# Kernel tuning notes

Measured on AMD Instinct MI355X. Metric: run time of the kernel, lower is better.

## Reference

```python
import jax, jax.numpy as jnp
import numpy as np

NBINS = 16  # init_kwargs nBins


def _next_fast_len(n):
    # smallest 5-smooth integer >= n (matches FastCMIF._nextFastLen)
    while True:
        m = n
        for p in (2, 3, 5):
            while m % p == 0:
                m //= p
        if m == 1:
            return n
        n += 1


def _normalize(im):
    mn = jnp.min(im, axis=(-2, -1), keepdims=True)
    mx = jnp.max(im, axis=(-2, -1), keepdims=True)
    return (im - mn) / (mx - mn)


def _one_hot(im):
    # (..., H, W) -> (..., NBINS, H, W)
    q = jnp.floor(im * (NBINS - 1)).astype(jnp.int32)
    return jnp.moveaxis(jax.nn.one_hot(q, NBINS, dtype=jnp.float32), -1, -3)


def _fftconv(im, template, padWl, padHt):
    s = (_next_fast_len(im.shape[-2] + template.shape[-2] - 1),
         _next_fast_len(im.shape[-1] + template.shape[-1] - 1))
    F = jnp.fft.rfft2(im, s=s) * jnp.fft.rfft2(jnp.flip(template, (-2, -1)), s=s)
    out = jnp.fft.irfft2(F, s=s)
    return out[..., padHt:padHt + im.shape[-2], padWl:padWl + im.shape[-1]]


def setup_inputs() -> dict:
    key = jax.random.key(0)
    k1, k2 = jax.random.split(key)
    im = jax.random.uniform(k1, (2, 1, 384, 384), dtype=jnp.float32)
    template = jax.random.uniform(k2, (2, 1, 48, 48), dtype=jnp.float32)
    return {"im": im, "template": template}


def reference(im, template):
    padWl = (template.shape[-1] - 1) // 2
    padHt = (template.shape[-2] - 1) // 2
    imOh = _one_hot(_normalize(im))            # (B,C,nBins,H,W)
    tOh = _one_hot(_normalize(template))       # (B,C,nBins,h,w)
    # marginal sliding-window histograms
    Px = _fftconv(imOh, jnp.ones_like(tOh), padWl, padHt)
    Py = _fftconv(jnp.ones_like(imOh), tOh, padWl, padHt)
    N = jnp.sum(Px, axis=-3, keepdims=True)    # (B,C,1,H,W)
    # joint sliding-window histogram (B,C,nBins,nBins,H,W)
    Pxy = _fftconv(imOh[..., :, None, :, :], tOh[..., None, :, :, :], padWl, padHt)
    Pxy = Pxy / N[..., None, :, :, :]
    Px = Px / N
    Py = Py / N
    # norm == "none": masked KL(Pxy || Px*Py)
    PxPy = Px[..., :, None, :, :] * Py[..., None, :, :, :]
    mask = (Pxy > 0) & (PxPy > 0)
    term = Pxy * (jnp.log(jnp.where(mask, Pxy, 1.0)) - jnp.log(jnp.where(mask, PxPy, 1.0)))
    return jnp.sum(jnp.where(mask, term, 0.0), axis=(-4, -3))  # (B,C,H,W)
```

## Files before the change

### kernel.cpp

```cpp
#include <hip/hip_runtime.h>


#define IMH 384
#define IMW 384
#define TH 48
#define TW 48
#define PAD 24
#define PH 432
#define PIMG (PH*PH)
#define NIMGW (PIMG/4)
#define TOTW (2*NIMGW)
#define FLTMAX 3.402823466e+38f
#define LN2F 0.69314718055994530942f

#if __has_builtin(__builtin_amdgcn_alignbyte)
#define ALIGNBYTE(hi,lo,s) __builtin_amdgcn_alignbyte((hi),(lo),(s))
#else
#define ALIGNBYTE(hi,lo,s) ((unsigned)(((((unsigned long long)(hi))<<32)|(unsigned long long)(lo)) >> ((s)*8)))
#endif

__global__ void k_mm1(const float* __restrict__ im, const float* __restrict__ tm,
                      unsigned* __restrict__ mnmx) {
    int b = blockIdx.x;
    const float* src;
    int base, cnt, g;
    if (b < 64) { src = im + (b >> 5) * (IMH*IMW); base = (b & 31) * 4608; cnt = 4608; g = b >> 5; }
    else        { src = tm + ((b - 64) >> 1) * (TH*TW); base = ((b - 64) & 1) * 1152; cnt = 1152; g = 2 + ((b - 64) >> 1); }
    float mn0 = FLTMAX, mx0 = -FLTMAX, mn1 = FLTMAX, mx1 = -FLTMAX;
    for (int i = threadIdx.x; i < cnt; i += 512) {
        float v = src[base + i];
        mn0 = fminf(mn0, v); mx0 = fmaxf(mx0, v);
        if (i + 256 < cnt) {
            float w = src[base + i + 256];
            mn1 = fminf(mn1, w); mx1 = fmaxf(mx1, w);
        }
    }
    float mn = fminf(mn0, mn1), mx = fmaxf(mx0, mx1);
    for (int o = 32; o > 0; o >>= 1) {
        mn = fminf(mn, __shfl_down(mn, o));
        mx = fmaxf(mx, __shfl_down(mx, o));
    }
    __shared__ float smn[4], smx[4];
    int w = threadIdx.x >> 6;
    if ((threadIdx.x & 63) == 0) { smn[w] = mn; smx[w] = mx; }
    __syncthreads();
    if (threadIdx.x == 0) {
        mn = fminf(fminf(smn[0], smn[1]), fminf(smn[2], smn[3]));
        mx = fmaxf(fmaxf(smx[0], smx[1]), fmaxf(smx[2], smx[3]));
        atomicMin(&mnmx[g],     __float_as_uint(mn));
        atomicMax(&mnmx[4 + g], __float_as_uint(mx));
    }
}

__global__ void k_prep(const float* __restrict__ im, const float* __restrict__ tm,
                       const unsigned* __restrict__ mm,
                       unsigned* __restrict__ pImW, unsigned* __restrict__ pT) {
    int blk = blockIdx.x;
    if (blk < 365) {
        int wi = blk * 256 + threadIdx.x;
        if (wi >= TOTW) return;
        int b = wi / NIMGW;
        int rem4 = (wi - b * NIMGW) * 4;
        int py = rem4 / PH;
        int px = rem4 - py * PH;
        float mn = __uint_as_float(mm[b]), mx = __uint_as_float(mm[4 + b]);
        unsigned word = 0;
        #pragma unroll
        for (int j = 0; j < 4; ++j) {
            int x = px + j;
            unsigned bin = 16u;
            if (py >= PAD && py < PAD + IMH && x >= PAD && x < PAD + IMW) {
                float v = im[b * (IMH*IMW) + (py - PAD) * IMW + (x - PAD)];
                float r = (v - mn) / (mx - mn);
                bin = (unsigned)(int)floorf(r * 15.0f);
            }
            word |= bin << (8*j);
        }
        pImW[wi] = word;
    } else {
        for (int t = threadIdx.x; t < 576; t += 256) {
            int b = t / 288, w = t - b * 288;
            float mn = __uint_as_float(mm[2 + b]), mx = __uint_as_float(mm[6 + b]);
            const float* tptr = tm + b * (TH*TW) + w * 8;
            unsigned word = 0;
            #pragma unroll
            for (int j = 0; j < 8; ++j) {
                float r = (tptr[j] - mn) / (mx - mn);
                word |= ((unsigned)(int)floorf(r * 15.0f)) << (4*j);
            }
            pT[b*288 + w] = word;
        }
    }
}

__device__ __forceinline__ void load_row(const uint2* rowp, int r, unsigned (&w)[14]) {
    const uint2* p = rowp + r * (PH / 8);
    #pragma unroll
    for (int i = 0; i < 7; ++i) { uint2 v = p[i]; w[2*i] = v.x; w[2*i+1] = v.y; }
}
__device__ __forceinline__ void load_t(const uint2* tp, int r, unsigned (&t)[6]) {
    const uint2* p = tp + r * 3;
    #pragma unroll
    for (int i = 0; i < 3; ++i) { uint2 v = p[i]; t[2*i] = v.x; t[2*i+1] = v.y; }
}

template<bool BORDER>
__device__ __forceinline__ void do_row(const unsigned (&w)[14], const unsigned (&t)[6],
                                       unsigned* __restrict__ hist, int tid,
                                       unsigned sh, bool sel) {
    unsigned wsel[13];
    #pragma unroll
    for (int i = 0; i < 13; ++i) wsel[i] = sel ? w[i+1] : w[i];
    unsigned a[12];
    #pragma unroll
    for (int i = 0; i < 12; ++i) a[i] = ALIGNBYTE(wsel[i+1], wsel[i], sh);
    unsigned tq[6];
    #pragma unroll
    for (int j = 0; j < 6; ++j)
        tq[j] = (unsigned)__builtin_amdgcn_readfirstlane((int)t[j]);

    #pragma unroll
    for (int c = 0; c < 48; ++c) {
        unsigned byteval = (a[c >> 2] >> ((c & 3) * 8)) & 0xFFu;
        unsigned l    = (tq[c >> 3] >> ((c & 7) * 4)) & 0xFu;
        unsigned soff = (l >> 2) << 6;
        unsigned sadd = 1u << ((l & 3u) << 3);
        if (BORDER) {
            unsigned bin   = byteval & 15u;
            unsigned adder = (byteval != 16u) ? sadd : 0u;
            atomicAdd(&hist[(bin << 8) + soff + tid], adder);
        } else {
            atomicAdd(&hist[(byteval << 8) + soff + tid], sadd);
        }
    }
}

template<bool BORDER>
__device__ __forceinline__ void accum_tile(const uint2* rowp, const uint2* tp,
                                           unsigned* __restrict__ hist, int tid,
                                           unsigned sh, bool sel) {
    unsigned w0[14], w1[14], t0[6], t1[6];
    load_row(rowp, 0, w0); load_t(tp, 0, t0);
    #pragma unroll 1
    for (int r = 0; r < 12; r += 2) {
        load_row(rowp, r + 1, w1); load_t(tp, r + 1, t1);
        do_row<BORDER>(w0, t0, hist, tid, sh, sel);
        if (r + 2 < 12) { load_row(rowp, r + 2, w0); load_t(tp, r + 2, t0); }
        do_row<BORDER>(w1, t1, hist, tid, sh, sel);
    }
}

__global__ __launch_bounds__(256, 4)
void k_main(const unsigned char* __restrict__ pIm, const unsigned* __restrict__ pT,
            float* __restrict__ out) {
    __shared__ unsigned hist[16 * 4 * 64];
    const int wv  = threadIdx.x >> 6;
    const int tid = threadIdx.x & 63;
    const int tx = tid & 7, ty = tid >> 3;
    const int b = blockIdx.z;
    const int X0 = blockIdx.x << 3, Y0 = blockIdx.y << 3;

    {
        uint4 z = {0u, 0u, 0u, 0u};
        #pragma unroll
        for (int i = 0; i < 4; ++i) ((uint4*)hist)[(wv * 4 + i) * 64 + tid] = z;
    }
    __syncthreads();

    const uint2* rowp = (const uint2*)(pIm + b * PIMG + (Y0 + ty + 12 * wv) * PH + X0);
    const uint2* tp   = (const uint2*)(pT + b * 288) + wv * 36;
    const unsigned sh = tx & 3;
    const bool sel = (tx & 4) != 0;

    const bool interior = (blockIdx.x >= 3) && (blockIdx.x <= 43) &&
                          (blockIdx.y >= 3) && (blockIdx.y <= 43);
    if (interior) accum_tile<false>(rowp, tp, hist, tid, sh, sel);
    else          accum_tile<true >(rowp, tp, hist, tid, sh, sel);

    __syncthreads();
    if (wv != 0) return;

    float A = 0.0f;
    int coll[16];
    #pragma unroll
    for (int i = 0; i < 16; ++i) coll[i] = 0;
    int N = 0;
    #pragma unroll
    for (int k = 0; k < 16; ++k) {
        int rk = 0;
        #pragma unroll
        for (int q = 0; q < 4; ++q) {
            unsigned v = hist[(k << 8) + (q << 6) + tid];
            #pragma unroll
            for (int j = 0; j < 4; ++j) {
                int c = (int)((v >> (8*j)) & 0xFFu);
                rk += c;
                coll[(q << 2) + j] += c;
                if (c) A += (float)c * __log2f((float)c);
            }
        }
        if (rk) A -= (float)rk * __log2f((float)rk);
        N += rk;
    }
    #pragma unroll
    for (int i = 0; i < 16; ++i)
        if (coll[i]) A -= (float)coll[i] * __log2f((float)coll[i]);
    float fN = (float)N;
    out[(b * IMH + Y0 + ty) * IMW + X0 + tx] = (A + fN * __log2f(fN)) * LN2F / fN;
}

extern "C" void kernel_launch(void* const* d_in, const int* in_sizes, int n_in,
                              void* d_out, int out_size, void* d_ws, size_t ws_size,
                              hipStream_t stream) {
    const float* im = (const float*)d_in[0];
    const float* tm = (const float*)d_in[1];
    float* out = (float*)d_out;
    unsigned char* pIm = (unsigned char*)d_ws;
    unsigned* pT   = (unsigned*)((char*)d_ws + 373248);
    unsigned* mnmx = (unsigned*)((char*)d_ws + 375552);

    hipMemsetAsync(mnmx, 0x7f, 16, stream);
    hipMemsetAsync((char*)mnmx + 16, 0x00, 16, stream);
    k_mm1<<<68, 256, 0, stream>>>(im, tm, mnmx);
    k_prep<<<366, 256, 0, stream>>>(im, tm, mnmx, (unsigned*)pIm, pT);
    k_main<<<dim3(48, 48, 2), 256, 0, stream>>>(pIm, pT, out);
}
```

Before: 199.9 us.

## Split histogram epilogue across all waves and drop memsets in min/max pass

The final entropy reduction in the main kernel now spreads the 16 joint-histogram rows over all four waves instead of one. Each wave computes its partial log-sum and column sums, and wave 0 combines them through shared memory. This adds a barrier and extra shared-memory traffic but cuts the serial epilogue per block. The min/max kernel now uses one 1024-thread block per image with float4 loads and writes results directly, which removes the two memset launches and the atomics at the cost of less parallelism in that pass.

```diff
diff --git a/kernel.cpp b/kernel.cpp
--- a/kernel.cpp
+++ b/kernel.cpp
@@ -19,36 +19,39 @@
 #define ALIGNBYTE(hi,lo,s) ((unsigned)(((((unsigned long long)(hi))<<32)|(unsigned long long)(lo)) >> ((s)*8)))
 #endif
 
-__global__ void k_mm1(const float* __restrict__ im, const float* __restrict__ tm,
-                      unsigned* __restrict__ mnmx) {
+__global__ __launch_bounds__(1024)
+void k_mm1(const float* __restrict__ im, const float* __restrict__ tm,
+           unsigned* __restrict__ mnmx) {
     int b = blockIdx.x;
-    const float* src;
-    int base, cnt, g;
-    if (b < 64) { src = im + (b >> 5) * (IMH*IMW); base = (b & 31) * 4608; cnt = 4608; g = b >> 5; }
-    else        { src = tm + ((b - 64) >> 1) * (TH*TW); base = ((b - 64) & 1) * 1152; cnt = 1152; g = 2 + ((b - 64) >> 1); }
-    float mn0 = FLTMAX, mx0 = -FLTMAX, mn1 = FLTMAX, mx1 = -FLTMAX;
-    for (int i = threadIdx.x; i < cnt; i += 512) {
-        float v = src[base + i];
-        mn0 = fminf(mn0, v); mx0 = fmaxf(mx0, v);
-        if (i + 256 < cnt) {
-            float w = src[base + i + 256];
-            mn1 = fminf(mn1, w); mx1 = fmaxf(mx1, w);
-        }
-    }
-    float mn = fminf(mn0, mn1), mx = fmaxf(mx0, mx1);
+    const float* src; int cnt;
+    if (b < 2) { src = im + b * (IMH*IMW); cnt = IMH*IMW; }
+    else       { src = tm + (b - 2) * (TH*TW); cnt = TH*TW; }
+    float mn = FLTMAX, mx = -FLTMAX;
+    const float4* s4 = (const float4*)src;
+    int n4 = cnt >> 2;
+    for (int i = threadIdx.x; i < n4; i += 1024) {
+        float4 v = s4[i];
+        mn = fminf(mn, fminf(fminf(v.x, v.y), fminf(v.z, v.w)));
+        mx = fmaxf(mx, fmaxf(fmaxf(v.x, v.y), fmaxf(v.z, v.w)));
+    }
     for (int o = 32; o > 0; o >>= 1) {
         mn = fminf(mn, __shfl_down(mn, o));
         mx = fmaxf(mx, __shfl_down(mx, o));
     }
-    __shared__ float smn[4], smx[4];
+    __shared__ float smn[16], smx[16];
     int w = threadIdx.x >> 6;
     if ((threadIdx.x & 63) == 0) { smn[w] = mn; smx[w] = mx; }
     __syncthreads();
-    if (threadIdx.x == 0) {
-        mn = fminf(fminf(smn[0], smn[1]), fminf(smn[2], smn[3]));
-        mx = fmaxf(fmaxf(smx[0], smx[1]), fmaxf(smx[2], smx[3]));
-        atomicMin(&mnmx[g],     __float_as_uint(mn));
-        atomicMax(&mnmx[4 + g], __float_as_uint(mx));
+    if (threadIdx.x < 16) {
+        mn = smn[threadIdx.x]; mx = smx[threadIdx.x];
+        for (int o = 8; o > 0; o >>= 1) {
+            mn = fminf(mn, __shfl_down(mn, o));
+            mx = fmaxf(mx, __shfl_down(mx, o));
+        }
+        if (threadIdx.x == 0) {
+            mnmx[b]     = __float_as_uint(mn);
+            mnmx[4 + b] = __float_as_uint(mx);
+        }
     }
 }
 
@@ -178,15 +181,14 @@
     else          accum_tile<true >(rowp, tp, hist, tid, sh, sel);
 
     __syncthreads();
-    if (wv != 0) return;
-
-    float A = 0.0f;
-    int coll[16];
-    #pragma unroll
-    for (int i = 0; i < 16; ++i) coll[i] = 0;
-    int N = 0;
-    #pragma unroll
-    for (int k = 0; k < 16; ++k) {
+
+    float Aw = 0.0f;
+    int colli[16];
+    #pragma unroll
+    for (int i = 0; i < 16; ++i) colli[i] = 0;
+    #pragma unroll
+    for (int kk = 0; kk < 4; ++kk) {
+        int k = (wv << 2) + kk;
         int rk = 0;
         #pragma unroll
         for (int q = 0; q < 4; ++q) {
@@ -195,16 +197,43 @@
             for (int j = 0; j < 4; ++j) {
                 int c = (int)((v >> (8*j)) & 0xFFu);
                 rk += c;
-                coll[(q << 2) + j] += c;
-                if (c) A += (float)c * __log2f((float)c);
+                colli[(q << 2) + j] += c;
+                if (c) Aw += (float)c * __log2f((float)c);
             }
         }
-        if (rk) A -= (float)rk * __log2f((float)rk);
-        N += rk;
-    }
-    #pragma unroll
-    for (int i = 0; i < 16; ++i)
+        if (rk) Aw -= (float)rk * __log2f((float)rk);
+    }
+    __syncthreads();
+
+    #pragma unroll
+    for (int j = 0; j < 8; ++j)
+        hist[(wv << 9) + (j << 6) + tid] =
+            (unsigned)colli[2*j] | ((unsigned)colli[2*j+1] << 16);
+    hist[2048 + (wv << 6) + tid] = __float_as_uint(Aw);
+    __syncthreads();
+    if (wv != 0) return;
+
+    float A = 0.0f;
+    #pragma unroll
+    for (int w = 0; w < 4; ++w) A += __uint_as_float(hist[2048 + (w << 6) + tid]);
+    int coll[16];
+    #pragma unroll
+    for (int i = 0; i < 16; ++i) coll[i] = 0;
+    #pragma unroll
+    for (int w = 0; w < 4; ++w) {
+        #pragma unroll
+        for (int j = 0; j < 8; ++j) {
+            unsigned u = hist[(w << 9) + (j << 6) + tid];
+            coll[2*j]   += (int)(u & 0xFFFFu);
+            coll[2*j+1] += (int)(u >> 16);
+        }
+    }
+    int N = 0;
+    #pragma unroll
+    for (int i = 0; i < 16; ++i) {
+        N += coll[i];
         if (coll[i]) A -= (float)coll[i] * __log2f((float)coll[i]);
+    }
     float fN = (float)N;
     out[(b * IMH + Y0 + ty) * IMW + X0 + tx] = (A + fN * __log2f(fN)) * LN2F / fN;
 }
@@ -219,9 +248,7 @@
     unsigned* pT   = (unsigned*)((char*)d_ws + 373248);
     unsigned* mnmx = (unsigned*)((char*)d_ws + 375552);
 
-    hipMemsetAsync(mnmx, 0x7f, 16, stream);
-    hipMemsetAsync((char*)mnmx + 16, 0x00, 16, stream);
-    k_mm1<<<68, 256, 0, stream>>>(im, tm, mnmx);
+    k_mm1<<<4, 1024, 0, stream>>>(im, tm, mnmx);
     k_prep<<<366, 256, 0, stream>>>(im, tm, mnmx, (unsigned*)pIm, pT);
     k_main<<<dim3(48, 48, 2), 256, 0, stream>>>(pIm, pT, out);
 }
```

After: 200.6 us. No clear change (+0.3%).
